# Kernel optimization log

Hardware: AMD Instinct MI355X
Metric: run time of the kernel (lower is better)

The kernel has to match this reference:

```python
import jax, jax.numpy as jnp
import numpy as np

N = 100000   # nodes
E = 1600000  # directed edges
HID = 64


def gat_conv(x, src, dst, W, a_src, a_dst, b, heads, out_ch):
    """PyG-style GATConv (add_self_loops=True, negative_slope=0.2, concat)."""
    n = x.shape[0]
    h = (x @ W).reshape(n, heads, out_ch)              # [N,H,C]
    loop = jnp.arange(n, dtype=src.dtype)
    s = jnp.concatenate([src, loop])                   # self loops appended
    d = jnp.concatenate([dst, loop])
    alpha_src = jnp.sum(h * a_src, axis=-1)            # [N,H]
    alpha_dst = jnp.sum(h * a_dst, axis=-1)            # [N,H]
    alpha = jax.nn.leaky_relu(alpha_src[s] + alpha_dst[d], 0.2)  # [E+N,H]
    # segment softmax over incoming edges of each destination node
    amax = jax.ops.segment_max(alpha, d, num_segments=n)
    alpha = jnp.exp(alpha - amax[d])
    asum = jax.ops.segment_sum(alpha, d, num_segments=n)
    alpha = alpha / (asum[d] + 1e-16)
    msg = h[s] * alpha[:, :, None]                     # [E+N,H,C]
    out = jax.ops.segment_sum(msg, d, num_segments=n)  # [N,H,C]
    return out.reshape(n, heads * out_ch) + b


def setup_inputs() -> dict:
    key = jax.random.key(0)
    ks = jax.random.split(key, 22)
    rn = lambda k, shp, s=0.1: (jax.random.normal(k, shp, jnp.float32) * s)
    inp = {
        "x": jax.random.normal(ks[0], (N, 2), jnp.float32),
        "edge_index": jax.random.randint(ks[1], (2, E), 0, N, dtype=jnp.int32),
        "edge_attr": jax.random.normal(ks[2], (E, 2), jnp.float32),
        # node encoder
        "enc_W": rn(ks[3], (2, HID)), "enc_b": rn(ks[4], (HID,)),
        # gat1: heads=4, out=16
        "g1_W": rn(ks[5], (HID, HID)), "g1_as": rn(ks[6], (4, 16)),
        "g1_ad": rn(ks[7], (4, 16)), "g1_b": rn(ks[8], (HID,)),
        # gat2: heads=1, out=64
        "g2_W": rn(ks[9], (HID, HID)), "g2_as": rn(ks[10], (1, HID)),
        "g2_ad": rn(ks[11], (1, HID)), "g2_b": rn(ks[12], (HID,)),
        # node head
        "no_W1": rn(ks[13], (HID, HID)), "no_b1": rn(ks[14], (HID,)),
        "no_W2": rn(ks[15], (HID, 2)), "no_b2": rn(ks[16], (2,)),
        # edge head: in = 2*HID + 2 = 130
        "eo_W1": rn(ks[17], (2 * HID + 2, HID)), "eo_b1": rn(ks[18], (HID,)),
        "eo_W2": rn(ks[19], (HID, 1)), "eo_b2": rn(ks[20], (1,)),
    }
    return inp


def reference(x, edge_index, edge_attr, enc_W, enc_b,
              g1_W, g1_as, g1_ad, g1_b,
              g2_W, g2_as, g2_ad, g2_b,
              no_W1, no_b1, no_W2, no_b2,
              eo_W1, eo_b1, eo_W2, eo_b2):
    src, dst = edge_index[0], edge_index[1]
    h = x @ enc_W + enc_b                                    # node encoder (dropout = eval identity)
    h = jax.nn.elu(gat_conv(h, src, dst, g1_W, g1_as, g1_ad, g1_b, 4, 16))
    h = gat_conv(h, src, dst, g2_W, g2_as, g2_ad, g2_b, 1, HID)
    e_in = jnp.concatenate([h[src], h[dst], edge_attr], axis=-1)  # [E,130]
    node_pred = jnp.tanh(jax.nn.leaky_relu(h @ no_W1 + no_b1, 0.01) @ no_W2 + no_b2)
    edge_pred = jnp.tanh(jax.nn.leaky_relu(e_in @ eo_W1 + eo_b1, 0.01) @ eo_W2 + eo_b2)[:, 0]
    return edge_pred, node_pred
```

## Files before the change

### kernel.cpp

```cpp
#include <hip/hip_runtime.h>
#include <hip/hip_fp16.h>
#include <math.h>


typedef _Float16 half8_t __attribute__((ext_vector_type(8)));
typedef float floatx4 __attribute__((ext_vector_type(4)));

__global__ void k_init_cursors(int* cursor, int NB, int cap){
  int b = blockIdx.x * blockDim.x + threadIdx.x;
  if (b < NB) cursor[b] = b * cap;
}

__global__ void k_scatter(const int* __restrict__ src, const int* __restrict__ dst,
                          int E, int NB, int cap, int* cursor,
                          unsigned int* __restrict__ ebuf){
  __shared__ int hist[256];
  __shared__ int base[256];
  int t = threadIdx.x;
  hist[t] = 0;
  __syncthreads();
  int cbase = blockIdx.x * 2048;
  int sv[8], bk[8], dl[8];
  #pragma unroll
  for (int i = 0; i < 8; ++i){
    int e = cbase + i * 256 + t;
    if (e < E){
      int d = dst[e];
      sv[i] = src[e]; bk[i] = d >> 9; dl[i] = d & 511;
      atomicAdd(&hist[bk[i]], 1);
    } else bk[i] = -1;
  }
  __syncthreads();
  int c = hist[t];
  base[t] = (t < NB && c > 0) ? atomicAdd(&cursor[t], c) : 0;
  __syncthreads();
  hist[t] = 0;
  __syncthreads();
  #pragma unroll
  for (int i = 0; i < 8; ++i){
    if (bk[i] >= 0){
      int r = atomicAdd(&hist[bk[i]], 1);
      int p = base[bk[i]] + r;
      if (p < (bk[i] + 1) * cap)
        ebuf[p] = (unsigned)sv[i] | ((unsigned)dl[i] << 17);
    }
  }
}

__global__ void k_bucket_build(const int* __restrict__ cursor, int cap, int N,
                               unsigned int* ebuf, int* __restrict__ rstart,
                               int* __restrict__ rend){
  __shared__ unsigned int ent[12288];
  __shared__ int cnts[512];
  __shared__ int aux[512];
  int b = blockIdx.x, t = threadIdx.x;
  int base = b * cap;
  int cnt = cursor[b] - base;
  if (cnt > cap) cnt = cap;
  for (int i = t; i < cnt; i += 512) ent[i] = ebuf[base + i];
  cnts[t] = 0;
  __syncthreads();
  for (int i = t; i < cnt; i += 512) atomicAdd(&cnts[ent[i] >> 17], 1);
  __syncthreads();
  int v = cnts[t];
  aux[t] = v;
  __syncthreads();
  for (int off = 1; off < 512; off <<= 1){
    int x = (t >= off) ? aux[t - off] : 0;
    __syncthreads();
    aux[t] += x;
    __syncthreads();
  }
  int incl = aux[t];
  int node = (b << 9) + t;
  if (node < N){ rstart[node] = base + incl - v; rend[node] = base + incl; }
  cnts[t] = incl - v;
  __syncthreads();
  for (int i = t; i < cnt; i += 512){
    unsigned int en = ent[i];
    int pos = atomicAdd(&cnts[en >> 17], 1);
    ebuf[base + pos] = en & 0x1FFFFu;
  }
}

__global__ void k_precompute(const float* __restrict__ encW, const float* __restrict__ encb,
                             const float* __restrict__ g1W, float* __restrict__ Mc){
  int j = threadIdx.x;
  if (j >= 64) return;
  float m0 = 0.f, m1 = 0.f, cc = 0.f;
  for (int t = 0; t < 64; ++t){
    float g = g1W[t * 64 + j];
    m0 = fmaf(encW[t], g, m0);
    m1 = fmaf(encW[64 + t], g, m1);
    cc = fmaf(encb[t], g, cc);
  }
  Mc[j] = m0; Mc[64 + j] = m1; Mc[128 + j] = cc;
}

__global__ void k_fuse1(const float* __restrict__ x, const float* __restrict__ Mc,
                        const float* __restrict__ a_s, const float* __restrict__ a_d,
                        __half* __restrict__ hw, float* __restrict__ alpha_s,
                        float* __restrict__ alpha_d, int n){
  int idx = blockIdx.x * blockDim.x + threadIdx.x;
  if (idx >= n * 64) return;
  int node = idx >> 6, j = idx & 63;
  float acc = fmaf(x[node * 2 + 0], Mc[j], fmaf(x[node * 2 + 1], Mc[64 + j], Mc[128 + j]));
  hw[idx] = __float2half(acc);
  float ps = acc * a_s[j];
  float pd = acc * a_d[j];
  #pragma unroll
  for (int off = 1; off < 16; off <<= 1){
    ps += __shfl_xor(ps, off);
    pd += __shfl_xor(pd, off);
  }
  if ((j & 15) == 0){
    int h = j >> 4;
    alpha_s[node * 4 + h] = ps;
    alpha_d[node * 4 + h] = pd;
  }
}

__global__ __launch_bounds__(256) void k_hw_mfma(
    const float* __restrict__ hin, const float* __restrict__ W,
    const float* __restrict__ a_s, const float* __restrict__ a_d,
    __half* __restrict__ hw, float* __restrict__ alpha_s,
    float* __restrict__ alpha_d, int n){
  __shared__ float redS[4][16];
  __shared__ float redD[4][16];
  int t = threadIdx.x;
  int lane = t & 63, wave = t >> 6;
  int l15 = lane & 15, quad = lane >> 4;
  int ch = wave * 16 + l15;
  half8_t b0, b1;
  #pragma unroll
  for (int j = 0; j < 8; ++j){
    b0[j] = (_Float16)W[(quad * 8 + j) * 64 + ch];
    b1[j] = (_Float16)W[(quad * 8 + j + 32) * 64 + ch];
  }
  float asv = a_s[ch], adv = a_d[ch];
  int base = blockIdx.x * 64;
  for (int it = 0; it < 4; ++it){
    int tb = base + it * 16;
    if (tb >= n) break;
    int arn = tb + l15; if (arn >= n) arn = n - 1;
    const float* arow = hin + (size_t)arn * 64 + quad * 8;
    half8_t a0, a1;
    #pragma unroll
    for (int j = 0; j < 8; ++j){
      a0[j] = (_Float16)arow[j];
      a1[j] = (_Float16)arow[j + 32];
    }
    floatx4 acc = {0.f, 0.f, 0.f, 0.f};
    acc = __builtin_amdgcn_mfma_f32_16x16x32_f16(a0, b0, acc, 0, 0, 0);
    acc = __builtin_amdgcn_mfma_f32_16x16x32_f16(a1, b1, acc, 0, 0, 0);
    float ps[4], pd[4];
    #pragma unroll
    for (int r = 0; r < 4; ++r){
      int node = tb + quad * 4 + r;
      if (node < n) hw[(size_t)node * 64 + ch] = __float2half(acc[r]);
      ps[r] = acc[r] * asv;
      pd[r] = acc[r] * adv;
      #pragma unroll
      for (int off = 1; off < 16; off <<= 1){
        ps[r] += __shfl_xor(ps[r], off);
        pd[r] += __shfl_xor(pd[r], off);
      }
    }
    if (l15 == 0){
      #pragma unroll
      for (int r = 0; r < 4; ++r){
        redS[wave][quad * 4 + r] = ps[r];
        redD[wave][quad * 4 + r] = pd[r];
      }
    }
    __syncthreads();
    if (t < 16 && tb + t < n){
      alpha_s[tb + t] = redS[0][t] + redS[1][t] + redS[2][t] + redS[3][t];
      alpha_d[tb + t] = redD[0][t] + redD[1][t] + redD[2][t] + redD[3][t];
    }
    __syncthreads();
  }
}

template<int H, bool ELU_ACT>
__global__ void k_agg(const __half* __restrict__ hw, const float* __restrict__ alpha_s,
                      const float* __restrict__ alpha_d, const int* __restrict__ rstart,
                      const int* __restrict__ rend, const int* __restrict__ col,
                      const float* __restrict__ bias, float* __restrict__ hout, int n){
  constexpr int C = 64 / H;
  int node = (blockIdx.x * blockDim.x + threadIdx.x) >> 6;
  int j = threadIdx.x & 63;
  if (node >= n) return;
  int h = j / C;
  int start = rstart[node], end = rend[node];
  float adn = alpha_d[node * H + h];
  float a_self = alpha_s[node * H + h] + adn;
  a_self = a_self > 0.f ? a_self : 0.2f * a_self;
  float psum, acc;
  {
    float p = __expf(a_self);
    psum = p;
    acc = p * __half2float(hw[node * 64 + j]);
  }
  int i = start;
  for (; i + 3 < end; i += 4){
    int s0 = col[i], s1 = col[i + 1], s2 = col[i + 2], s3 = col[i + 3];
    float a0 = alpha_s[s0 * H + h] + adn;
    float a1 = alpha_s[s1 * H + h] + adn;
    float a2 = alpha_s[s2 * H + h] + adn;
    float a3 = alpha_s[s3 * H + h] + adn;
    float w0 = __half2float(hw[s0 * 64 + j]);
    float w1 = __half2float(hw[s1 * 64 + j]);
    float w2 = __half2float(hw[s2 * 64 + j]);
    float w3 = __half2float(hw[s3 * 64 + j]);
    a0 = a0 > 0.f ? a0 : 0.2f * a0;
    a1 = a1 > 0.f ? a1 : 0.2f * a1;
    a2 = a2 > 0.f ? a2 : 0.2f * a2;
    a3 = a3 > 0.f ? a3 : 0.2f * a3;
    float p0 = __expf(a0), p1 = __expf(a1), p2 = __expf(a2), p3 = __expf(a3);
    psum += (p0 + p1) + (p2 + p3);
    acc = fmaf(p0, w0, fmaf(p1, w1, fmaf(p2, w2, fmaf(p3, w3, acc))));
  }
  for (; i < end; ++i){
    int s = col[i];
    float a = alpha_s[s * H + h] + adn;
    a = a > 0.f ? a : 0.2f * a;
    float p = __expf(a);
    psum += p;
    acc = fmaf(p, __half2float(hw[s * 64 + j]), acc);
  }
  float o = acc / (psum + 1e-16f) + bias[j];
  if (ELU_ACT) o = o > 0.f ? o : (__expf(o) - 1.f);
  hout[node * 64 + j] = o;
}

__global__ __launch_bounds__(256) void k_heads_mfma(
    const float* __restrict__ h, const float* __restrict__ eoW1,
    const float* __restrict__ noW1, const float* __restrict__ nob1,
    const float* __restrict__ noW2, const float* __restrict__ nob2,
    __half* __restrict__ P1, __half* __restrict__ P2,
    float* __restrict__ outN, int n){
  __shared__ float redP[4][16][2];
  int t = threadIdx.x;
  int lane = t & 63, wave = t >> 6;
  int l15 = lane & 15, quad = lane >> 4;
  int ch = wave * 16 + l15;
  half8_t bP1a, bP1b, bP2a, bP2b, bNa, bNb;
  #pragma unroll
  for (int j = 0; j < 8; ++j){
    int k0 = quad * 8 + j, k1 = k0 + 32;
    bP1a[j] = (_Float16)eoW1[k0 * 64 + ch];
    bP1b[j] = (_Float16)eoW1[k1 * 64 + ch];
    bP2a[j] = (_Float16)eoW1[(k0 + 64) * 64 + ch];
    bP2b[j] = (_Float16)eoW1[(k1 + 64) * 64 + ch];
    bNa[j]  = (_Float16)noW1[k0 * 64 + ch];
    bNb[j]  = (_Float16)noW1[k1 * 64 + ch];
  }
  float b1v = nob1[ch];
  float w20 = noW2[ch * 2 + 0], w21 = noW2[ch * 2 + 1];
  float b20 = nob2[0], b21 = nob2[1];
  int base = blockIdx.x * 64;
  for (int it = 0; it < 4; ++it){
    int tb = base + it * 16;
    if (tb >= n) break;
    int arn = tb + l15; if (arn >= n) arn = n - 1;
    const float* arow = h + (size_t)arn * 64 + quad * 8;
    half8_t a0, a1;
    #pragma unroll
    for (int j = 0; j < 8; ++j){
      a0[j] = (_Float16)arow[j];
      a1[j] = (_Float16)arow[j + 32];
    }
    floatx4 ac1 = {0.f,0.f,0.f,0.f}, ac2 = {0.f,0.f,0.f,0.f}, acN = {0.f,0.f,0.f,0.f};
    ac1 = __builtin_amdgcn_mfma_f32_16x16x32_f16(a0, bP1a, ac1, 0, 0, 0);
    ac1 = __builtin_amdgcn_mfma_f32_16x16x32_f16(a1, bP1b, ac1, 0, 0, 0);
    ac2 = __builtin_amdgcn_mfma_f32_16x16x32_f16(a0, bP2a, ac2, 0, 0, 0);
    ac2 = __builtin_amdgcn_mfma_f32_16x16x32_f16(a1, bP2b, ac2, 0, 0, 0);
    acN = __builtin_amdgcn_mfma_f32_16x16x32_f16(a0, bNa, acN, 0, 0, 0);
    acN = __builtin_amdgcn_mfma_f32_16x16x32_f16(a1, bNb, acN, 0, 0, 0);
    float p0[4], p1[4];
    #pragma unroll
    for (int r = 0; r < 4; ++r){
      int node = tb + quad * 4 + r;
      if (node < n){
        P1[(size_t)node * 64 + ch] = __float2half(ac1[r]);
        P2[(size_t)node * 64 + ch] = __float2half(ac2[r]);
      }
      float v = acN[r] + b1v;
      v = v > 0.f ? v : 0.01f * v;
      p0[r] = v * w20;
      p1[r] = v * w21;
      #pragma unroll
      for (int off = 1; off < 16; off <<= 1){
        p0[r] += __shfl_xor(p0[r], off);
        p1[r] += __shfl_xor(p1[r], off);
      }
    }
    if (l15 == 0){
      #pragma unroll
      for (int r = 0; r < 4; ++r){
        redP[wave][quad * 4 + r][0] = p0[r];
        redP[wave][quad * 4 + r][1] = p1[r];
      }
    }
    __syncthreads();
    if (t < 16 && tb + t < n){
      float s0 = redP[0][t][0] + redP[1][t][0] + redP[2][t][0] + redP[3][t][0];
      float s1 = redP[0][t][1] + redP[1][t][1] + redP[2][t][1] + redP[3][t][1];
      outN[(size_t)(tb + t) * 2 + 0] = tanhf(s0 + b20);
      outN[(size_t)(tb + t) * 2 + 1] = tanhf(s1 + b21);
    }
    __syncthreads();
  }
}

__global__ void k_edge_head(const __half* __restrict__ P1h, const __half* __restrict__ P2h,
                            const int* __restrict__ src, const int* __restrict__ dst,
                            const float* __restrict__ eattr, const float* __restrict__ eoW1,
                            const float* __restrict__ b1, const float* __restrict__ W2,
                            const float* __restrict__ b2, float* __restrict__ out, int E){
  int lane = threadIdx.x & 63;
  int jj = lane & 7, q = lane >> 3;
  int wid = (blockIdx.x * blockDim.x + threadIdx.x) >> 6;
  int nw = (gridDim.x * blockDim.x) >> 6;

  const float4* rAq = (const float4*)(eoW1 + 8192);
  const float4* rBq = (const float4*)(eoW1 + 8256);
  const float4* b1q = (const float4*)b1;
  const float4* w2q = (const float4*)W2;
  float4 tA0 = rAq[2 * jj], tA1 = rAq[2 * jj + 1];
  float4 tB0 = rBq[2 * jj], tB1 = rBq[2 * jj + 1];
  float4 tb0 = b1q[2 * jj], tb1 = b1q[2 * jj + 1];
  float4 tw0 = w2q[2 * jj], tw1 = w2q[2 * jj + 1];
  float ra[8] = {tA0.x, tA0.y, tA0.z, tA0.w, tA1.x, tA1.y, tA1.z, tA1.w};
  float rb[8] = {tB0.x, tB0.y, tB0.z, tB0.w, tB1.x, tB1.y, tB1.z, tB1.w};
  float bb[8] = {tb0.x, tb0.y, tb0.z, tb0.w, tb1.x, tb1.y, tb1.z, tb1.w};
  float w2[8] = {tw0.x, tw0.y, tw0.z, tw0.w, tw1.x, tw1.y, tw1.z, tw1.w};
  float b2v = b2[0];

  const float4* P1q = (const float4*)P1h;
  const float4* P2q = (const float4*)P2h;
  const float2* eav = (const float2*)eattr;

  int groups = (E + 7) >> 3;
  for (int g = wid; g < groups; g += nw){
    int e = g * 8 + q;
    bool act = (e < E);
    float p = 0.f;
    if (act){
      int s = src[e], d = dst[e];
      float2 ea = eav[e];
      float4 g1 = P1q[(size_t)s * 8 + jj];
      float4 g2 = P2q[(size_t)d * 8 + jj];
      const __half2* h1 = (const __half2*)&g1;
      const __half2* h2 = (const __half2*)&g2;
      float v[8];
      #pragma unroll
      for (int k = 0; k < 4; ++k){
        float2 u = __half22float2(h1[k]);
        float2 w = __half22float2(h2[k]);
        v[2 * k]     = u.x + w.x;
        v[2 * k + 1] = u.y + w.y;
      }
      #pragma unroll
      for (int k = 0; k < 8; ++k){
        float t = v[k] + bb[k];
        t = fmaf(ea.x, ra[k], fmaf(ea.y, rb[k], t));
        t = t > 0.f ? t : 0.01f * t;
        p = fmaf(t, w2[k], p);
      }
    }
    #pragma unroll
    for (int off = 1; off < 8; off <<= 1) p += __shfl_xor(p, off);
    if (jj == 0 && act) out[e] = tanhf(p + b2v);
  }
}

extern "C" void kernel_launch(void* const* d_in, const int* in_sizes, int n_in,
                              void* d_out, int out_size, void* d_ws, size_t ws_size,
                              hipStream_t stream){
  const float* x    = (const float*)d_in[0];
  const int*   eidx = (const int*)  d_in[1];
  const float* ea   = (const float*)d_in[2];
  const float* encW = (const float*)d_in[3];
  const float* encb = (const float*)d_in[4];
  const float* g1W  = (const float*)d_in[5];
  const float* g1as = (const float*)d_in[6];
  const float* g1ad = (const float*)d_in[7];
  const float* g1b  = (const float*)d_in[8];
  const float* g2W  = (const float*)d_in[9];
  const float* g2as = (const float*)d_in[10];
  const float* g2ad = (const float*)d_in[11];
  const float* g2b  = (const float*)d_in[12];
  const float* noW1 = (const float*)d_in[13];
  const float* nob1 = (const float*)d_in[14];
  const float* noW2 = (const float*)d_in[15];
  const float* nob2 = (const float*)d_in[16];
  const float* eoW1 = (const float*)d_in[17];
  const float* eob1 = (const float*)d_in[18];
  const float* eoW2 = (const float*)d_in[19];
  const float* eob2 = (const float*)d_in[20];

  const int N = in_sizes[0] / 2;
  const int E = in_sizes[1] / 2;
  const int* src = eidx;
  const int* dst = eidx + E;

  const int NB = (N + 511) >> 9;
  int avg = (E + NB - 1) / NB;
  int cap = avg + avg / 4 + 64;
  if (cap > 12288) cap = 12288;

  char* ws = (char*)d_ws;
  size_t off = 0;
  auto alloc = [&](size_t bytes) -> void* {
    void* p = ws + off;
    off = (off + bytes + 255) & ~(size_t)255;
    return p;
  };
  float*  bufA  = (float*) alloc((size_t)N * 64 * 4);
  __half* bufH  = (__half*)alloc((size_t)N * 64 * 2);
  __half* P1h   = (__half*)alloc((size_t)N * 64 * 2);
  __half* P2h   = (__half*)alloc((size_t)N * 64 * 2);
  float*  as    = (float*) alloc((size_t)N * 4 * 4);
  float*  ad    = (float*) alloc((size_t)N * 4 * 4);
  int* rstart   = (int*)   alloc((size_t)N * 4);
  int* rend     = (int*)   alloc((size_t)N * 4);
  unsigned int* ebuf = (unsigned int*)alloc((size_t)NB * cap * 4);
  int* cursor   = (int*)   alloc((size_t)NB * 4);
  float* Mc     = (float*) alloc(192 * 4);

  k_init_cursors<<<(NB + 255) / 256, 256, 0, stream>>>(cursor, NB, cap);
  k_scatter<<<(E + 2047) / 2048, 256, 0, stream>>>(src, dst, E, NB, cap, cursor, ebuf);
  k_bucket_build<<<NB, 512, 0, stream>>>(cursor, cap, N, ebuf, rstart, rend);
  const int* col = (const int*)ebuf;

  k_precompute<<<1, 64, 0, stream>>>(encW, encb, g1W, Mc);
  k_fuse1<<<(N * 64 + 255) / 256, 256, 0, stream>>>(x, Mc, g1as, g1ad, bufH, as, ad, N);
  k_agg<4, true><<<(N * 64 + 255) / 256, 256, 0, stream>>>(bufH, as, ad, rstart, rend, col, g1b, bufA, N);

  k_hw_mfma<<<(N + 63) / 64, 256, 0, stream>>>(bufA, g2W, g2as, g2ad, bufH, as, ad, N);
  k_agg<1, false><<<(N * 64 + 255) / 256, 256, 0, stream>>>(bufH, as, ad, rstart, rend, col, g2b, bufA, N);

  float* out = (float*)d_out;
  k_heads_mfma<<<(N + 63) / 64, 256, 0, stream>>>(bufA, eoW1, noW1, nob1, noW2, nob2,
                                                  P1h, P2h, out + E, N);
  k_edge_head<<<2048, 256, 0, stream>>>(P1h, P2h, src, dst, ea,
                                        eoW1, eob1, eoW2, eob2, out, E);
}
```

Before: 408.8 us.

## Split GAT aggregation wave into four edge groups with vectorized half loads

Each 64-lane wave still handles one node, but lanes are now split into four groups of 16. Each group walks every fourth incoming edge, and each lane loads four half channels with one 8-byte load and keeps four fp32 accumulators. Partial sums are combined with cross-group shuffles, and group 0 writes a float4 output. This raises memory-level parallelism and load width for the gathers in exchange for shuffle reductions and idle lanes in the epilogue; the grid size is unchanged.

```diff
diff --git a/kernel.cpp b/kernel.cpp
--- a/kernel.cpp
+++ b/kernel.cpp
@@ -187,51 +187,62 @@
                       const float* __restrict__ alpha_d, const int* __restrict__ rstart,
                       const int* __restrict__ rend, const int* __restrict__ col,
                       const float* __restrict__ bias, float* __restrict__ hout, int n){
-  constexpr int C = 64 / H;
   int node = (blockIdx.x * blockDim.x + threadIdx.x) >> 6;
-  int j = threadIdx.x & 63;
+  int lane = threadIdx.x & 63;
+  int g = lane >> 4, c = lane & 15;
   if (node >= n) return;
-  int h = j / C;
+  int hidx = (c * H) >> 4;
+  float adn = alpha_d[node * H + hidx];
   int start = rstart[node], end = rend[node];
-  float adn = alpha_d[node * H + h];
-  float a_self = alpha_s[node * H + h] + adn;
-  a_self = a_self > 0.f ? a_self : 0.2f * a_self;
-  float psum, acc;
-  {
-    float p = __expf(a_self);
-    psum = p;
-    acc = p * __half2float(hw[node * 64 + j]);
-  }
-  int i = start;
-  for (; i + 3 < end; i += 4){
-    int s0 = col[i], s1 = col[i + 1], s2 = col[i + 2], s3 = col[i + 3];
-    float a0 = alpha_s[s0 * H + h] + adn;
-    float a1 = alpha_s[s1 * H + h] + adn;
-    float a2 = alpha_s[s2 * H + h] + adn;
-    float a3 = alpha_s[s3 * H + h] + adn;
-    float w0 = __half2float(hw[s0 * 64 + j]);
-    float w1 = __half2float(hw[s1 * 64 + j]);
-    float w2 = __half2float(hw[s2 * 64 + j]);
-    float w3 = __half2float(hw[s3 * 64 + j]);
-    a0 = a0 > 0.f ? a0 : 0.2f * a0;
-    a1 = a1 > 0.f ? a1 : 0.2f * a1;
-    a2 = a2 > 0.f ? a2 : 0.2f * a2;
-    a3 = a3 > 0.f ? a3 : 0.2f * a3;
-    float p0 = __expf(a0), p1 = __expf(a1), p2 = __expf(a2), p3 = __expf(a3);
-    psum += (p0 + p1) + (p2 + p3);
-    acc = fmaf(p0, w0, fmaf(p1, w1, fmaf(p2, w2, fmaf(p3, w3, acc))));
-  }
-  for (; i < end; ++i){
-    int s = col[i];
-    float a = alpha_s[s * H + h] + adn;
+  float acc0 = 0.f, acc1 = 0.f, acc2 = 0.f, acc3 = 0.f, psum = 0.f;
+  if (g == 0){
+    float a = alpha_s[node * H + hidx] + adn;
     a = a > 0.f ? a : 0.2f * a;
     float p = __expf(a);
+    psum = p;
+    float2 rv = *(const float2*)(hw + (size_t)node * 64 + c * 4);
+    const __half2* hp = (const __half2*)&rv;
+    float2 f0 = __half22float2(hp[0]), f1 = __half22float2(hp[1]);
+    acc0 = p * f0.x; acc1 = p * f0.y; acc2 = p * f1.x; acc3 = p * f1.y;
+  }
+  for (int i = start + g; i < end; i += 4){
+    int s = col[i];
+    float a = alpha_s[s * H + hidx] + adn;
+    a = a > 0.f ? a : 0.2f * a;
+    float p = __expf(a);
+    float2 rv = *(const float2*)(hw + (size_t)s * 64 + c * 4);
+    const __half2* hp = (const __half2*)&rv;
+    float2 f0 = __half22float2(hp[0]), f1 = __half22float2(hp[1]);
     psum += p;
-    acc = fmaf(p, __half2float(hw[s * 64 + j]), acc);
-  }
-  float o = acc / (psum + 1e-16f) + bias[j];
-  if (ELU_ACT) o = o > 0.f ? o : (__expf(o) - 1.f);
-  hout[node * 64 + j] = o;
+    acc0 = fmaf(p, f0.x, acc0);
+    acc1 = fmaf(p, f0.y, acc1);
+    acc2 = fmaf(p, f1.x, acc2);
+    acc3 = fmaf(p, f1.y, acc3);
+  }
+  #pragma unroll
+  for (int off = 16; off < 64; off <<= 1){
+    psum += __shfl_xor(psum, off);
+    acc0 += __shfl_xor(acc0, off);
+    acc1 += __shfl_xor(acc1, off);
+    acc2 += __shfl_xor(acc2, off);
+    acc3 += __shfl_xor(acc3, off);
+  }
+  if (g == 0){
+    float inv = 1.f / (psum + 1e-16f);
+    float4 bv = ((const float4*)bias)[c];
+    float o0 = fmaf(acc0, inv, bv.x);
+    float o1 = fmaf(acc1, inv, bv.y);
+    float o2 = fmaf(acc2, inv, bv.z);
+    float o3 = fmaf(acc3, inv, bv.w);
+    if (ELU_ACT){
+      o0 = o0 > 0.f ? o0 : (__expf(o0) - 1.f);
+      o1 = o1 > 0.f ? o1 : (__expf(o1) - 1.f);
+      o2 = o2 > 0.f ? o2 : (__expf(o2) - 1.f);
+      o3 = o3 > 0.f ? o3 : (__expf(o3) - 1.f);
+    }
+    float4 ov = {o0, o1, o2, o3};
+    *(float4*)(hout + (size_t)node * 64 + c * 4) = ov;
+  }
 }
 
 __global__ __launch_bounds__(256) void k_heads_mfma(
@@ -437,10 +448,10 @@
 
   k_precompute<<<1, 64, 0, stream>>>(encW, encb, g1W, Mc);
   k_fuse1<<<(N * 64 + 255) / 256, 256, 0, stream>>>(x, Mc, g1as, g1ad, bufH, as, ad, N);
-  k_agg<4, true><<<(N * 64 + 255) / 256, 256, 0, stream>>>(bufH, as, ad, rstart, rend, col, g1b, bufA, N);
+  k_agg<4, true><<<(N + 3) / 4, 256, 0, stream>>>(bufH, as, ad, rstart, rend, col, g1b, bufA, N);
 
   k_hw_mfma<<<(N + 63) / 64, 256, 0, stream>>>(bufA, g2W, g2as, g2ad, bufH, as, ad, N);
-  k_agg<1, false><<<(N * 64 + 255) / 256, 256, 0, stream>>>(bufH, as, ad, rstart, rend, col, g2b, bufA, N);
+  k_agg<1, false><<<(N + 3) / 4, 256, 0, stream>>>(bufH, as, ad, rstart, rend, col, g2b, bufA, N);
 
   float* out = (float*)d_out;
   k_heads_mfma<<<(N + 63) / 64, 256, 0, stream>>>(bufA, eoW1, noW1, nob1, noW2, nob2,
```

Result: faster. 398.4 us (-2.5%).
